# Performance work log

Measured on AMD Instinct MI355X. Metric: run time of the kernel, lower is better.

## Reference

```python
import jax, jax.numpy as jnp
import numpy as np

# Static graph / model sizes (closed over; match input_specs)
N0, N1, N2 = 500_000, 100_000, 25_000   # nodes per hop (targets are prefix of sources)
E0, E1 = 1_600_000, 400_000             # edges per hop
D_IN, D_H, D_OUT = 128, 256, 128


def setup_inputs() -> dict:
    key = jax.random.key(0)
    ks = jax.random.split(key, 11)
    s_in = 1.0 / np.sqrt(D_IN)
    s_h = 1.0 / np.sqrt(D_H)
    return {
        "x": jax.random.normal(ks[0], (N0, D_IN), dtype=jnp.float32),
        # layer 0 params (SAGEConv in->hidden): lin_l (with bias) on aggregated, lin_r (no bias) on root
        "W_l0": jax.random.normal(ks[1], (D_H, D_IN), dtype=jnp.float32) * s_in,
        "b_l0": jax.random.normal(ks[2], (D_H,), dtype=jnp.float32) * s_in,
        "W_r0": jax.random.normal(ks[3], (D_H, D_IN), dtype=jnp.float32) * s_in,
        # layer 1 params (SAGEConv hidden->out)
        "W_l1": jax.random.normal(ks[4], (D_OUT, D_H), dtype=jnp.float32) * s_h,
        "b_l1": jax.random.normal(ks[5], (D_OUT,), dtype=jnp.float32) * s_h,
        "W_r1": jax.random.normal(ks[6], (D_OUT, D_H), dtype=jnp.float32) * s_h,
        # bipartite edge indices: src in [0, N_src), dst in [0, N_dst)
        "ei0_src": jax.random.randint(ks[7], (E0,), 0, N0),
        "ei0_dst": jax.random.randint(ks[8], (E0,), 0, N1),
        "ei1_src": jax.random.randint(ks[9], (E1,), 0, N1),
        "ei1_dst": jax.random.randint(ks[10], (E1,), 0, N2),
    }


def _sage_conv(x_src, x_dst, src, dst, n_dst, W_l, b_l, W_r):
    """PyG SAGEConv, aggr='mean': lin_l(mean_neigh) + lin_r(x_dst)."""
    msg = x_src[src]                                                # [E, d] gather
    agg = jax.ops.segment_sum(msg, dst, num_segments=n_dst)        # [n_dst, d]
    cnt = jax.ops.segment_sum(jnp.ones((src.shape[0],), msg.dtype), dst,
                              num_segments=n_dst)                  # [n_dst]
    agg = agg / jnp.clip(cnt, 1.0)[:, None]                        # mean (safe for isolated nodes)
    return agg @ W_l.T + b_l + x_dst @ W_r.T


def reference(x, W_l0, b_l0, W_r0, W_l1, b_l1, W_r1,
              ei0_src, ei0_dst, ei1_src, ei1_dst):
    # hop 0: targets are first N1 rows of x
    h = _sage_conv(x, x[:N1], ei0_src, ei0_dst, N1, W_l0, b_l0, W_r0)
    h = jax.nn.relu(h)  # relu on all but last layer
    # hop 1 (last layer, no relu)
    out = _sage_conv(h, h[:N2], ei1_src, ei1_dst, N2, W_l1, b_l1, W_r1)
    return out
```

## Files before the change

### kernel.cpp

```cpp
#include <hip/hip_runtime.h>
#include <hip/hip_bf16.h>

#define cN0 500000
#define cN1 100000
#define cN2 25000
#define cE0 1600000
#define cE1 400000

typedef __bf16 bf16x8 __attribute__((ext_vector_type(8)));
typedef __bf16 bf16x4 __attribute__((ext_vector_type(4)));
typedef float f32x4 __attribute__((ext_vector_type(4)));

__global__ __launch_bounds__(256) void k_prep(
    const float* __restrict__ x, __bf16* __restrict__ xb,
    const int* __restrict__ e0d, int* __restrict__ off0,
    const int* __restrict__ e1d, int* __restrict__ off1,
    const float* __restrict__ Wl0, const float* __restrict__ Wr0, __bf16* __restrict__ Wc0,
    const float* __restrict__ Wl1, const float* __restrict__ Wr1, __bf16* __restrict__ Wc1)
{
    const int b = blockIdx.x;
    const int t = threadIdx.x;
    if (b < 31250) {
        const int i = b * 256 + t;
        const float4 v0 = *(const float4*)(x + (size_t)i * 8);
        const float4 v1 = *(const float4*)(x + (size_t)i * 8 + 4);
        bf16x8 o;
        o[0] = (__bf16)v0.x; o[1] = (__bf16)v0.y; o[2] = (__bf16)v0.z; o[3] = (__bf16)v0.w;
        o[4] = (__bf16)v1.x; o[5] = (__bf16)v1.y; o[6] = (__bf16)v1.z; o[7] = (__bf16)v1.w;
        *(bf16x8*)(xb + (size_t)i * 8) = o;
    } else if (b < 37500) {
        const int i = (b - 31250) * 256 + t;
        atomicAdd(&off0[e0d[i]], 1);
    } else if (b < 39063) {
        const int i = (b - 37500) * 256 + t;
        if (i < cE1) atomicAdd(&off1[e1d[i]], 1);
    } else if (b < 39319) {
        const int i = (b - 39063) * 256 + t;
        const int j = i >> 8, k = i & 255;
        float v = (k < 128) ? Wl0[j * 128 + k] : Wr0[j * 128 + (k - 128)];
        Wc0[i] = (__bf16)v;
    } else {
        const int i = (b - 39319) * 256 + t;
        const int j = i >> 9, k = i & 511;
        float v = (k < 256) ? Wl1[j * 256 + k] : Wr1[j * 256 + (k - 256)];
        Wc1[i] = (__bf16)v;
    }
}

__global__ void k_scanA(int* __restrict__ off0, int* __restrict__ bsum0,
                        int* __restrict__ off1, int* __restrict__ bsum1) {
    __shared__ int lds[256];
    const int t = threadIdx.x;
    int* a; int n; int* bsum; int blk;
    if (blockIdx.x < 98) { a = off0; n = cN1; bsum = bsum0; blk = blockIdx.x; }
    else                 { a = off1; n = cN2; bsum = bsum1; blk = blockIdx.x - 98; }
    const int base = blk * 1024 + t * 4;
    int v0 = (base + 0 < n) ? a[base + 0] : 0;
    int v1 = (base + 1 < n) ? a[base + 1] : 0;
    int v2 = (base + 2 < n) ? a[base + 2] : 0;
    int v3 = (base + 3 < n) ? a[base + 3] : 0;
    const int s = v0 + v1 + v2 + v3;
    lds[t] = s;
    __syncthreads();
    int x = s;
    for (int d = 1; d < 256; d <<= 1) {
        int y = (t >= d) ? lds[t - d] : 0;
        __syncthreads();
        x += y;
        lds[t] = x;
        __syncthreads();
    }
    if (t == 255) bsum[blk] = x;
    int e0 = x - s;
    int e1 = e0 + v0, e2 = e1 + v1, e3 = e2 + v2;
    if (base + 0 < n) a[base + 0] = e0;
    if (base + 1 < n) a[base + 1] = e1;
    if (base + 2 < n) a[base + 2] = e2;
    if (base + 3 < n) a[base + 3] = e3;
}

__global__ void k_scanB(int* __restrict__ bsum0, int* __restrict__ bsum1) {
    __shared__ int lds[128];
    const int t = threadIdx.x;
    int* bsum = (blockIdx.x == 0) ? bsum0 : bsum1;
    const int nb = (blockIdx.x == 0) ? 98 : 25;
    int v = (t < nb) ? bsum[t] : 0;
    lds[t] = v;
    __syncthreads();
    int x = v;
    for (int d = 1; d < 128; d <<= 1) {
        int y = (t >= d) ? lds[t - d] : 0;
        __syncthreads();
        x += y;
        lds[t] = x;
        __syncthreads();
    }
    if (t < nb) bsum[t] = x - v;
}

__global__ void k_scanC(int* __restrict__ off0, const int* __restrict__ bsum0, int* __restrict__ cur0,
                        int* __restrict__ off1, const int* __restrict__ bsum1, int* __restrict__ cur1) {
    int* a; const int* bsum; int* cur; int n, total, blk;
    if (blockIdx.x < 391) { a = off0; bsum = bsum0; cur = cur0; n = cN1; total = cE0; blk = blockIdx.x; }
    else                  { a = off1; bsum = bsum1; cur = cur1; n = cN2; total = cE1; blk = blockIdx.x - 391; }
    const int i = blk * 256 + threadIdx.x;
    if (i < n) {
        int v = a[i] + bsum[i >> 10];
        a[i] = v;
        cur[i] = v;
    }
    if (i == 0) a[n] = total;
}

__global__ void k_scatter2(const int* __restrict__ e0s, const int* __restrict__ e0d,
                           int* __restrict__ cur0, int* __restrict__ srcs0,
                           const int* __restrict__ e1s, const int* __restrict__ e1d,
                           int* __restrict__ cur1, int* __restrict__ srcs1) {
    if (blockIdx.x < 6250) {
        const int i = blockIdx.x * 256 + threadIdx.x;
        const int p = atomicAdd(&cur0[e0d[i]], 1);
        srcs0[p] = e0s[i];
    } else {
        const int i = (blockIdx.x - 6250) * 256 + threadIdx.x;
        if (i < cE1) {
            const int p = atomicAdd(&cur1[e1d[i]], 1);
            srcs1[p] = e1s[i];
        }
    }
}

__global__ __launch_bounds__(256) void k_agg0(
    const __bf16* __restrict__ xb,
    const int* __restrict__ off, const int* __restrict__ srcs,
    const __bf16* __restrict__ zrow,
    __bf16* __restrict__ Agg)
{
    const int wid = blockIdx.x * 4 + (threadIdx.x >> 6);
    const int lane = threadIdx.x & 63;
    const int slot = lane >> 4;
    const int dl = lane & 15;
    const int gbase = wid * 8;
    for (int n = 0; n < 8; ++n) {
        const int g = gbase + n;
        if (g >= cN1) return;
        const int e0 = off[g], e1 = off[g + 1];
        const int deg = e1 - e0;
        float a[8] = {0.f, 0.f, 0.f, 0.f, 0.f, 0.f, 0.f, 0.f};
        const int iters = (deg + 3) >> 2;
        for (int it = 0; it < iters; ++it) {
            const int e = e0 + it * 4 + slot;
            const __bf16* rp = zrow;
            if (e < e1) rp = xb + (size_t)srcs[e] * 128;
            const bf16x8 r = *(const bf16x8*)(rp + dl * 8);
            #pragma unroll
            for (int d = 0; d < 8; ++d) a[d] += (float)r[d];
        }
        #pragma unroll
        for (int d = 0; d < 8; ++d) {
            a[d] += __shfl_xor(a[d], 16);
            a[d] += __shfl_xor(a[d], 32);
        }
        if (slot == 0) {
            const float inv = 1.f / (float)(deg > 0 ? deg : 1);
            bf16x8 o;
            #pragma unroll
            for (int d = 0; d < 8; ++d) o[d] = (__bf16)(a[d] * inv);
            *(bf16x8*)(Agg + (size_t)g * 128 + dl * 8) = o;
        }
    }
}

__global__ __launch_bounds__(256) void k_agg1(
    const __bf16* __restrict__ h,
    const int* __restrict__ off, const int* __restrict__ srcs,
    const __bf16* __restrict__ zrow,
    __bf16* __restrict__ Agg)
{
    const int wid = blockIdx.x * 4 + (threadIdx.x >> 6);
    const int lane = threadIdx.x & 63;
    const int slot = lane >> 5;
    const int dl = lane & 31;
    const int gbase = wid * 4;
    for (int n = 0; n < 4; ++n) {
        const int g = gbase + n;
        if (g >= cN2) return;
        const int e0 = off[g], e1 = off[g + 1];
        const int deg = e1 - e0;
        float a[8] = {0.f, 0.f, 0.f, 0.f, 0.f, 0.f, 0.f, 0.f};
        const int iters = (deg + 1) >> 1;
        for (int it = 0; it < iters; ++it) {
            const int e = e0 + it * 2 + slot;
            const __bf16* rp = zrow;
            if (e < e1) rp = h + (size_t)srcs[e] * 256;
            const bf16x8 r = *(const bf16x8*)(rp + dl * 8);
            #pragma unroll
            for (int d = 0; d < 8; ++d) a[d] += (float)r[d];
        }
        #pragma unroll
        for (int d = 0; d < 8; ++d) a[d] += __shfl_xor(a[d], 32);
        if (slot == 0) {
            const float inv = 1.f / (float)(deg > 0 ? deg : 1);
            bf16x8 o;
            #pragma unroll
            for (int d = 0; d < 8; ++d) o[d] = (__bf16)(a[d] * inv);
            *(bf16x8*)(Agg + (size_t)g * 256 + dl * 8) = o;
        }
    }
}

template<int KHALF, int LDC, bool RELU, bool OUTBF16>
__global__ __launch_bounds__(256) void k_gemm(
    const __bf16* __restrict__ A1, const __bf16* __restrict__ A2,
    const __bf16* __restrict__ W, const float* __restrict__ bias,
    float* __restrict__ outf, __bf16* __restrict__ outb, int Mrows)
{
    const int K = KHALF * 2;
    const int tid = threadIdx.x;
    const int l = tid & 63;
    const int w = tid >> 6;
    const int wm = w & 1, wn = w >> 1;
    const int row0 = blockIdx.x * 128 + wm * 64;
    const int col0 = blockIdx.y * 128 + wn * 64;
    const int lr = l & 15;
    const int lk = (l >> 4) * 8;

    const __bf16* pa1[4];
    const __bf16* pa2[4];
    const __bf16* pb[4];
    #pragma unroll
    for (int i = 0; i < 4; ++i) {
        int r = row0 + i * 16 + lr;
        r = (r < Mrows) ? r : (Mrows - 1);
        pa1[i] = A1 + (size_t)r * KHALF + lk;
        pa2[i] = A2 + (size_t)r * KHALF + lk;
        pb[i] = W + (size_t)(col0 + i * 16 + lr) * K + lk;
    }
    f32x4 acc[4][4];
    #pragma unroll
    for (int i = 0; i < 4; ++i)
        #pragma unroll
        for (int j = 0; j < 4; ++j)
            acc[i][j] = (f32x4)0.0f;

    #pragma unroll 2
    for (int k0 = 0; k0 < KHALF; k0 += 32) {
        bf16x8 fa[4], fb[4];
        #pragma unroll
        for (int i = 0; i < 4; ++i) fa[i] = *(const bf16x8*)(pa1[i] + k0);
        #pragma unroll
        for (int j = 0; j < 4; ++j) fb[j] = *(const bf16x8*)(pb[j] + k0);
        #pragma unroll
        for (int i = 0; i < 4; ++i)
            #pragma unroll
            for (int j = 0; j < 4; ++j)
                acc[i][j] = __builtin_amdgcn_mfma_f32_16x16x32_bf16(fa[i], fb[j], acc[i][j], 0, 0, 0);
    }
    #pragma unroll 2
    for (int k0 = 0; k0 < KHALF; k0 += 32) {
        bf16x8 fa[4], fb[4];
        #pragma unroll
        for (int i = 0; i < 4; ++i) fa[i] = *(const bf16x8*)(pa2[i] + k0);
        #pragma unroll
        for (int j = 0; j < 4; ++j) fb[j] = *(const bf16x8*)(pb[j] + KHALF + k0);
        #pragma unroll
        for (int i = 0; i < 4; ++i)
            #pragma unroll
            for (int j = 0; j < 4; ++j)
                acc[i][j] = __builtin_amdgcn_mfma_f32_16x16x32_bf16(fa[i], fb[j], acc[i][j], 0, 0, 0);
    }

    #pragma unroll
    for (int j = 0; j < 4; ++j) {
        const int colg = col0 + j * 16 + lr;
        const float bj = bias[colg];
        #pragma unroll
        for (int i = 0; i < 4; ++i) {
            #pragma unroll
            for (int reg = 0; reg < 4; ++reg) {
                const int rowg = row0 + i * 16 + (l >> 4) * 4 + reg;
                if (rowg < Mrows) {
                    float v = acc[i][j][reg] + bj;
                    if (RELU) v = fmaxf(v, 0.f);
                    if (OUTBF16) outb[(size_t)rowg * LDC + colg] = (__bf16)v;
                    else         outf[(size_t)rowg * LDC + colg] = v;
                }
            }
        }
    }
}


extern "C" void kernel_launch(void* const* d_in, const int* in_sizes, int n_in,
                              void* d_out, int out_size, void* d_ws, size_t ws_size,
                              hipStream_t stream) {
    const float* x   = (const float*)d_in[0];
    const float* Wl0 = (const float*)d_in[1];
    const float* bl0 = (const float*)d_in[2];
    const float* Wr0 = (const float*)d_in[3];
    const float* Wl1 = (const float*)d_in[4];
    const float* bl1 = (const float*)d_in[5];
    const float* Wr1 = (const float*)d_in[6];
    const int* e0s = (const int*)d_in[7];
    const int* e0d = (const int*)d_in[8];
    const int* e1s = (const int*)d_in[9];
    const int* e1d = (const int*)d_in[10];
    float* out = (float*)d_out;

    char* ws = (char*)d_ws;
    size_t pos = 0;
    auto alloc = [&](size_t nb) -> void* {
        void* p = ws + pos;
        pos += (nb + 255) & ~(size_t)255;
        return p;
    };
    __bf16* xb   = (__bf16*)alloc((size_t)cN0 * 128 * 2);
    __bf16* h    = (__bf16*)alloc((size_t)cN1 * 256 * 2);
    __bf16* Agg0 = (__bf16*)alloc((size_t)cN1 * 128 * 2);
    __bf16* Agg1 = Agg0;
    int* off0    = (int*)alloc(((size_t)(cN1 + 1) + (cN2 + 1) + 128) * 4);
    int* off1    = off0 + (cN1 + 1);
    __bf16* zrow = (__bf16*)(off1 + (cN2 + 1));
    const size_t zbytes = ((size_t)(cN1 + 1) + (cN2 + 1) + 128) * 4;
    int* cur0    = (int*)alloc((size_t)cN1 * 4);
    int* srcs0   = (int*)alloc((size_t)cE0 * 4);
    int* cur1    = (int*)alloc((size_t)cN2 * 4);
    int* srcs1   = (int*)alloc((size_t)cE1 * 4);
    int* bsum0   = (int*)alloc(128 * 4);
    int* bsum1   = (int*)alloc(128 * 4);
    __bf16* Wc0  = (__bf16*)alloc(256 * 256 * 2);
    __bf16* Wc1  = (__bf16*)alloc(128 * 512 * 2);
    (void)ws_size; (void)in_sizes; (void)n_in; (void)out_size;

    hipMemsetAsync(off0, 0, zbytes, stream);
    k_prep<<<39575, 256, 0, stream>>>(x, xb, e0d, off0, e1d, off1,
                                      Wl0, Wr0, Wc0, Wl1, Wr1, Wc1);
    k_scanA<<<123, 256, 0, stream>>>(off0, bsum0, off1, bsum1);
    k_scanB<<<2, 128, 0, stream>>>(bsum0, bsum1);
    k_scanC<<<489, 256, 0, stream>>>(off0, bsum0, cur0, off1, bsum1, cur1);
    k_scatter2<<<7813, 256, 0, stream>>>(e0s, e0d, cur0, srcs0, e1s, e1d, cur1, srcs1);

    k_agg0<<<(cN1 + 31) / 32, 256, 0, stream>>>(xb, off0, srcs0, zrow, Agg0);
    {
        dim3 grid((cN1 + 127) / 128, 2);
        k_gemm<128, 256, true, true><<<grid, 256, 0, stream>>>(Agg0, xb, Wc0, bl0, nullptr, h, cN1);
    }
    k_agg1<<<(cN2 + 15) / 16, 256, 0, stream>>>(h, off1, srcs1, zrow, Agg1);
    {
        dim3 grid((cN2 + 127) / 128, 1);
        k_gemm<256, 128, false, false><<<grid, 256, 0, stream>>>(Agg1, h, Wc1, bl1, out, nullptr, cN2);
    }
}
```

Measured before the change: 850.5 us.

## Build CSR via two-level bucketed sort and aggregate two nodes per wave

Replaces the per-destination atomic histogram and scatter with a coarse 16-node bucket histogram, then a per-bucket block that sorts edges into CSR order using shared-memory atomics. The goal is to cut global atomic contention and the scattered srcs writes, at the cost of an extra pass over an int2 pair array. The aggregation kernels now process two destination nodes at once so more gather loads are in flight; this removes the per-node bounds check, which is safe only because the node counts divide evenly.

```diff
diff --git a/kernel.cpp b/kernel.cpp
--- a/kernel.cpp
+++ b/kernel.cpp
@@ -6,15 +6,16 @@
 #define cN2 25000
 #define cE0 1600000
 #define cE1 400000
+#define NB0 6250
+#define NB1 1563
 
 typedef __bf16 bf16x8 __attribute__((ext_vector_type(8)));
-typedef __bf16 bf16x4 __attribute__((ext_vector_type(4)));
 typedef float f32x4 __attribute__((ext_vector_type(4)));
 
 __global__ __launch_bounds__(256) void k_prep(
     const float* __restrict__ x, __bf16* __restrict__ xb,
-    const int* __restrict__ e0d, int* __restrict__ off0,
-    const int* __restrict__ e1d, int* __restrict__ off1,
+    const int* __restrict__ e0d, int* __restrict__ bkt0,
+    const int* __restrict__ e1d, int* __restrict__ bkt1,
     const float* __restrict__ Wl0, const float* __restrict__ Wr0, __bf16* __restrict__ Wc0,
     const float* __restrict__ Wl1, const float* __restrict__ Wr1, __bf16* __restrict__ Wc1)
 {
@@ -30,10 +31,10 @@
         *(bf16x8*)(xb + (size_t)i * 8) = o;
     } else if (b < 37500) {
         const int i = (b - 31250) * 256 + t;
-        atomicAdd(&off0[e0d[i]], 1);
+        atomicAdd(&bkt0[e0d[i] >> 4], 1);
     } else if (b < 39063) {
         const int i = (b - 37500) * 256 + t;
-        if (i < cE1) atomicAdd(&off1[e1d[i]], 1);
+        if (i < cE1) atomicAdd(&bkt1[e1d[i] >> 4], 1);
     } else if (b < 39319) {
         const int i = (b - 39063) * 256 + t;
         const int j = i >> 8, k = i & 255;
@@ -47,13 +48,13 @@
     }
 }
 
-__global__ void k_scanA(int* __restrict__ off0, int* __restrict__ bsum0,
-                        int* __restrict__ off1, int* __restrict__ bsum1) {
+__global__ void k_scanA(int* __restrict__ bkt0, int* __restrict__ bsum0,
+                        int* __restrict__ bkt1, int* __restrict__ bsum1) {
     __shared__ int lds[256];
     const int t = threadIdx.x;
     int* a; int n; int* bsum; int blk;
-    if (blockIdx.x < 98) { a = off0; n = cN1; bsum = bsum0; blk = blockIdx.x; }
-    else                 { a = off1; n = cN2; bsum = bsum1; blk = blockIdx.x - 98; }
+    if (blockIdx.x < 7) { a = bkt0; n = NB0; bsum = bsum0; blk = blockIdx.x; }
+    else                { a = bkt1; n = NB1; bsum = bsum1; blk = blockIdx.x - 7; }
     const int base = blk * 1024 + t * 4;
     int v0 = (base + 0 < n) ? a[base + 0] : 0;
     int v1 = (base + 1 < n) ? a[base + 1] : 0;
@@ -83,7 +84,7 @@
     __shared__ int lds[128];
     const int t = threadIdx.x;
     int* bsum = (blockIdx.x == 0) ? bsum0 : bsum1;
-    const int nb = (blockIdx.x == 0) ? 98 : 25;
+    const int nb = (blockIdx.x == 0) ? 7 : 2;
     int v = (t < nb) ? bsum[t] : 0;
     lds[t] = v;
     __syncthreads();
@@ -98,11 +99,11 @@
     if (t < nb) bsum[t] = x - v;
 }
 
-__global__ void k_scanC(int* __restrict__ off0, const int* __restrict__ bsum0, int* __restrict__ cur0,
-                        int* __restrict__ off1, const int* __restrict__ bsum1, int* __restrict__ cur1) {
+__global__ void k_scanC(int* __restrict__ bkt0, const int* __restrict__ bsum0, int* __restrict__ bcur0,
+                        int* __restrict__ bkt1, const int* __restrict__ bsum1, int* __restrict__ bcur1) {
     int* a; const int* bsum; int* cur; int n, total, blk;
-    if (blockIdx.x < 391) { a = off0; bsum = bsum0; cur = cur0; n = cN1; total = cE0; blk = blockIdx.x; }
-    else                  { a = off1; bsum = bsum1; cur = cur1; n = cN2; total = cE1; blk = blockIdx.x - 391; }
+    if (blockIdx.x < 25) { a = bkt0; bsum = bsum0; cur = bcur0; n = NB0; total = cE0; blk = blockIdx.x; }
+    else                 { a = bkt1; bsum = bsum1; cur = bcur1; n = NB1; total = cE1; blk = blockIdx.x - 25; }
     const int i = blk * 256 + threadIdx.x;
     if (i < n) {
         int v = a[i] + bsum[i >> 10];
@@ -112,20 +113,56 @@
     if (i == 0) a[n] = total;
 }
 
-__global__ void k_scatter2(const int* __restrict__ e0s, const int* __restrict__ e0d,
-                           int* __restrict__ cur0, int* __restrict__ srcs0,
-                           const int* __restrict__ e1s, const int* __restrict__ e1d,
-                           int* __restrict__ cur1, int* __restrict__ srcs1) {
+__global__ void k_phaseB(const int* __restrict__ e0s, const int* __restrict__ e0d,
+                         int* __restrict__ bcur0, int2* __restrict__ pair0,
+                         const int* __restrict__ e1s, const int* __restrict__ e1d,
+                         int* __restrict__ bcur1, int2* __restrict__ pair1) {
     if (blockIdx.x < 6250) {
         const int i = blockIdx.x * 256 + threadIdx.x;
-        const int p = atomicAdd(&cur0[e0d[i]], 1);
-        srcs0[p] = e0s[i];
+        const int d = e0d[i];
+        const int p = atomicAdd(&bcur0[d >> 4], 1);
+        pair0[p] = make_int2(e0s[i], d);
     } else {
         const int i = (blockIdx.x - 6250) * 256 + threadIdx.x;
         if (i < cE1) {
-            const int p = atomicAdd(&cur1[e1d[i]], 1);
-            srcs1[p] = e1s[i];
-        }
+            const int d = e1d[i];
+            const int p = atomicAdd(&bcur1[d >> 4], 1);
+            pair1[p] = make_int2(e1s[i], d);
+        }
+    }
+}
+
+__global__ __launch_bounds__(256) void k_phaseC(
+    const int* __restrict__ boff0, const int2* __restrict__ pair0,
+    int* __restrict__ off0, int* __restrict__ srcs0,
+    const int* __restrict__ boff1, const int2* __restrict__ pair1,
+    int* __restrict__ off1, int* __restrict__ srcs1) {
+    __shared__ int deg[16], pre[16], cur[16];
+    const int t = threadIdx.x;
+    const int* boff; const int2* pr; int* off; int* srcs; int bkt, ndst, Etot;
+    if (blockIdx.x < NB0) { bkt = blockIdx.x;       boff = boff0; pr = pair0; off = off0; srcs = srcs0; ndst = cN1; Etot = cE0; }
+    else                  { bkt = blockIdx.x - NB0; boff = boff1; pr = pair1; off = off1; srcs = srcs1; ndst = cN2; Etot = cE1; }
+    const int p0 = boff[bkt], p1 = boff[bkt + 1];
+    const int cnt = p1 - p0;
+    if (t < 16) deg[t] = 0;
+    __syncthreads();
+    for (int i = t; i < cnt; i += 256) atomicAdd(&deg[pr[p0 + i].y & 15], 1);
+    __syncthreads();
+    if (t == 0) {
+        int s = 0;
+        #pragma unroll
+        for (int l = 0; l < 16; ++l) { pre[l] = s; cur[l] = s; s += deg[l]; }
+    }
+    __syncthreads();
+    if (t < 16) {
+        const int d = bkt * 16 + t;
+        if (d < ndst) off[d] = p0 + pre[t];
+    }
+    if (t == 0 && bkt == 0) off[ndst] = Etot;
+    for (int i = t; i < cnt; i += 256) {
+        const int2 e = pr[p0 + i];
+        const int p = atomicAdd(&cur[e.y & 15], 1);
+        srcs[p0 + p] = e.x;
     }
 }
 
@@ -140,32 +177,46 @@
     const int slot = lane >> 4;
     const int dl = lane & 15;
     const int gbase = wid * 8;
-    for (int n = 0; n < 8; ++n) {
-        const int g = gbase + n;
-        if (g >= cN1) return;
-        const int e0 = off[g], e1 = off[g + 1];
-        const int deg = e1 - e0;
-        float a[8] = {0.f, 0.f, 0.f, 0.f, 0.f, 0.f, 0.f, 0.f};
-        const int iters = (deg + 3) >> 2;
-        for (int it = 0; it < iters; ++it) {
-            const int e = e0 + it * 4 + slot;
-            const __bf16* rp = zrow;
-            if (e < e1) rp = xb + (size_t)srcs[e] * 128;
-            const bf16x8 r = *(const bf16x8*)(rp + dl * 8);
-            #pragma unroll
-            for (int d = 0; d < 8; ++d) a[d] += (float)r[d];
+    for (int n = 0; n < 8; n += 2) {
+        const int ga = gbase + n, gb = gbase + n + 1;
+        const int a0 = off[ga], a1 = off[ga + 1];
+        const int b0 = off[gb], b1 = off[gb + 1];
+        float aa[8] = {0.f,0.f,0.f,0.f,0.f,0.f,0.f,0.f};
+        float ab[8] = {0.f,0.f,0.f,0.f,0.f,0.f,0.f,0.f};
+        const int ita = (a1 - a0 + 3) >> 2;
+        const int itb = (b1 - b0 + 3) >> 2;
+        const int it = (ita > itb) ? ita : itb;
+        for (int i2 = 0; i2 < it; ++i2) {
+            const int ea = a0 + i2 * 4 + slot;
+            const int eb = b0 + i2 * 4 + slot;
+            const __bf16* pa = (ea < a1) ? xb + (size_t)srcs[ea] * 128 : zrow;
+            const __bf16* pb = (eb < b1) ? xb + (size_t)srcs[eb] * 128 : zrow;
+            const bf16x8 ra = *(const bf16x8*)(pa + dl * 8);
+            const bf16x8 rb = *(const bf16x8*)(pb + dl * 8);
+            #pragma unroll
+            for (int d = 0; d < 8; ++d) { aa[d] += (float)ra[d]; ab[d] += (float)rb[d]; }
         }
         #pragma unroll
         for (int d = 0; d < 8; ++d) {
-            a[d] += __shfl_xor(a[d], 16);
-            a[d] += __shfl_xor(a[d], 32);
+            aa[d] += __shfl_xor(aa[d], 16);
+            aa[d] += __shfl_xor(aa[d], 32);
+            ab[d] += __shfl_xor(ab[d], 16);
+            ab[d] += __shfl_xor(ab[d], 32);
         }
         if (slot == 0) {
+            const int deg = a1 - a0;
             const float inv = 1.f / (float)(deg > 0 ? deg : 1);
             bf16x8 o;
             #pragma unroll
-            for (int d = 0; d < 8; ++d) o[d] = (__bf16)(a[d] * inv);
-            *(bf16x8*)(Agg + (size_t)g * 128 + dl * 8) = o;
+            for (int d = 0; d < 8; ++d) o[d] = (__bf16)(aa[d] * inv);
+            *(bf16x8*)(Agg + (size_t)ga * 128 + dl * 8) = o;
+        } else if (slot == 1) {
+            const int deg = b1 - b0;
+            const float inv = 1.f / (float)(deg > 0 ? deg : 1);
+            bf16x8 o;
+            #pragma unroll
+            for (int d = 0; d < 8; ++d) o[d] = (__bf16)(ab[d] * inv);
+            *(bf16x8*)(Agg + (size_t)gb * 128 + dl * 8) = o;
         }
     }
 }
@@ -181,29 +232,45 @@
     const int slot = lane >> 5;
     const int dl = lane & 31;
     const int gbase = wid * 4;
-    for (int n = 0; n < 4; ++n) {
-        const int g = gbase + n;
-        if (g >= cN2) return;
-        const int e0 = off[g], e1 = off[g + 1];
-        const int deg = e1 - e0;
-        float a[8] = {0.f, 0.f, 0.f, 0.f, 0.f, 0.f, 0.f, 0.f};
-        const int iters = (deg + 1) >> 1;
-        for (int it = 0; it < iters; ++it) {
-            const int e = e0 + it * 2 + slot;
-            const __bf16* rp = zrow;
-            if (e < e1) rp = h + (size_t)srcs[e] * 256;
-            const bf16x8 r = *(const bf16x8*)(rp + dl * 8);
-            #pragma unroll
-            for (int d = 0; d < 8; ++d) a[d] += (float)r[d];
-        }
-        #pragma unroll
-        for (int d = 0; d < 8; ++d) a[d] += __shfl_xor(a[d], 32);
+    if (gbase >= cN2) return;
+    for (int n = 0; n < 4; n += 2) {
+        const int ga = gbase + n, gb = gbase + n + 1;
+        const int a0 = off[ga], a1 = off[ga + 1];
+        const int b0 = off[gb], b1 = off[gb + 1];
+        float aa[8] = {0.f,0.f,0.f,0.f,0.f,0.f,0.f,0.f};
+        float ab[8] = {0.f,0.f,0.f,0.f,0.f,0.f,0.f,0.f};
+        const int ita = (a1 - a0 + 1) >> 1;
+        const int itb = (b1 - b0 + 1) >> 1;
+        const int it = (ita > itb) ? ita : itb;
+        for (int i2 = 0; i2 < it; ++i2) {
+            const int ea = a0 + i2 * 2 + slot;
+            const int eb = b0 + i2 * 2 + slot;
+            const __bf16* pa = (ea < a1) ? h + (size_t)srcs[ea] * 256 : zrow;
+            const __bf16* pb = (eb < b1) ? h + (size_t)srcs[eb] * 256 : zrow;
+            const bf16x8 ra = *(const bf16x8*)(pa + dl * 8);
+            const bf16x8 rb = *(const bf16x8*)(pb + dl * 8);
+            #pragma unroll
+            for (int d = 0; d < 8; ++d) { aa[d] += (float)ra[d]; ab[d] += (float)rb[d]; }
+        }
+        #pragma unroll
+        for (int d = 0; d < 8; ++d) {
+            aa[d] += __shfl_xor(aa[d], 32);
+            ab[d] += __shfl_xor(ab[d], 32);
+        }
         if (slot == 0) {
+            const int deg = a1 - a0;
             const float inv = 1.f / (float)(deg > 0 ? deg : 1);
             bf16x8 o;
             #pragma unroll
-            for (int d = 0; d < 8; ++d) o[d] = (__bf16)(a[d] * inv);
-            *(bf16x8*)(Agg + (size_t)g * 256 + dl * 8) = o;
+            for (int d = 0; d < 8; ++d) o[d] = (__bf16)(aa[d] * inv);
+            *(bf16x8*)(Agg + (size_t)ga * 256 + dl * 8) = o;
+        } else {
+            const int deg = b1 - b0;
+            const float inv = 1.f / (float)(deg > 0 ? deg : 1);
+            bf16x8 o;
+            #pragma unroll
+            for (int d = 0; d < 8; ++d) o[d] = (__bf16)(ab[d] * inv);
+            *(bf16x8*)(Agg + (size_t)gb * 256 + dl * 8) = o;
         }
     }
 }
@@ -317,13 +384,17 @@
     __bf16* h    = (__bf16*)alloc((size_t)cN1 * 256 * 2);
     __bf16* Agg0 = (__bf16*)alloc((size_t)cN1 * 128 * 2);
     __bf16* Agg1 = Agg0;
-    int* off0    = (int*)alloc(((size_t)(cN1 + 1) + (cN2 + 1) + 128) * 4);
-    int* off1    = off0 + (cN1 + 1);
-    __bf16* zrow = (__bf16*)(off1 + (cN2 + 1));
-    const size_t zbytes = ((size_t)(cN1 + 1) + (cN2 + 1) + 128) * 4;
-    int* cur0    = (int*)alloc((size_t)cN1 * 4);
+    int* bkt0    = (int*)alloc(((size_t)(NB0 + 1) + (NB1 + 1) + 128) * 4);
+    int* bkt1    = bkt0 + (NB0 + 1);
+    __bf16* zrow = (__bf16*)(bkt1 + (NB1 + 1));
+    const size_t zbytes = ((size_t)(NB0 + 1) + (NB1 + 1) + 128) * 4;
+    int* bcur0   = (int*)alloc((size_t)NB0 * 4);
+    int* bcur1   = (int*)alloc((size_t)NB1 * 4);
+    int2* pair0  = (int2*)alloc((size_t)cE0 * 8);
+    int2* pair1  = (int2*)alloc((size_t)cE1 * 8);
+    int* off0    = (int*)alloc((size_t)(cN1 + 1) * 4);
+    int* off1    = (int*)alloc((size_t)(cN2 + 1) * 4);
     int* srcs0   = (int*)alloc((size_t)cE0 * 4);
-    int* cur1    = (int*)alloc((size_t)cN2 * 4);
     int* srcs1   = (int*)alloc((size_t)cE1 * 4);
     int* bsum0   = (int*)alloc(128 * 4);
     int* bsum1   = (int*)alloc(128 * 4);
@@ -331,20 +402,22 @@
     __bf16* Wc1  = (__bf16*)alloc(128 * 512 * 2);
     (void)ws_size; (void)in_sizes; (void)n_in; (void)out_size;
 
-    hipMemsetAsync(off0, 0, zbytes, stream);
-    k_prep<<<39575, 256, 0, stream>>>(x, xb, e0d, off0, e1d, off1,
+    hipMemsetAsync(bkt0, 0, zbytes, stream);
+    k_prep<<<39575, 256, 0, stream>>>(x, xb, e0d, bkt0, e1d, bkt1,
                                       Wl0, Wr0, Wc0, Wl1, Wr1, Wc1);
-    k_scanA<<<123, 256, 0, stream>>>(off0, bsum0, off1, bsum1);
+    k_scanA<<<9, 256, 0, stream>>>(bkt0, bsum0, bkt1, bsum1);
     k_scanB<<<2, 128, 0, stream>>>(bsum0, bsum1);
-    k_scanC<<<489, 256, 0, stream>>>(off0, bsum0, cur0, off1, bsum1, cur1);
-    k_scatter2<<<7813, 256, 0, stream>>>(e0s, e0d, cur0, srcs0, e1s, e1d, cur1, srcs1);
-
-    k_agg0<<<(cN1 + 31) / 32, 256, 0, stream>>>(xb, off0, srcs0, zrow, Agg0);
+    k_scanC<<<32, 256, 0, stream>>>(bkt0, bsum0, bcur0, bkt1, bsum1, bcur1);
+    k_phaseB<<<7813, 256, 0, stream>>>(e0s, e0d, bcur0, pair0, e1s, e1d, bcur1, pair1);
+    k_phaseC<<<NB0 + NB1, 256, 0, stream>>>(bkt0, pair0, off0, srcs0,
+                                            bkt1, pair1, off1, srcs1);
+
+    k_agg0<<<3125, 256, 0, stream>>>(xb, off0, srcs0, zrow, Agg0);
     {
         dim3 grid((cN1 + 127) / 128, 2);
         k_gemm<128, 256, true, true><<<grid, 256, 0, stream>>>(Agg0, xb, Wc0, bl0, nullptr, h, cN1);
     }
-    k_agg1<<<(cN2 + 15) / 16, 256, 0, stream>>>(h, off1, srcs1, zrow, Agg1);
+    k_agg1<<<(6250 + 3) / 4, 256, 0, stream>>>(h, off1, srcs1, zrow, Agg1);
     {
         dim3 grid((cN2 + 127) / 128, 1);
         k_gemm<256, 128, false, false><<<grid, 256, 0, stream>>>(Agg1, h, Wc1, bl1, out, nullptr, cN2);
```

Result: no change. 836.9 us (-1.6%).
